# Performance work log

Measured on AMD Instinct MI355X. Metric: run time of the kernel, lower is better.

The kernel has to match this reference:

```python
import jax, jax.numpy as jnp
import numpy as np

B, T, HID = 2, 2048, 2048
NH = 8
D = HID // NH  # head_dim = 256 (expand_ratio=1 so input_dim == hidden_size)
EPS_RMS = 1e-8   # RMSNorm inside BitLinear
EPS_LN = 1e-5    # layernorm_eps for g_norm


def _rms(x, w, eps):
    # weighted RMSNorm over last dim
    return x * jax.lax.rsqrt(jnp.mean(x * x, axis=-1, keepdims=True) + eps) * w


def _act_quant(x):
    # per-token 8-bit fake quant with straight-through estimator
    s = 127.0 / jnp.clip(jnp.max(jnp.abs(x), axis=-1, keepdims=True), 1e-5)
    q = jnp.clip(jnp.round(x * s), -128, 127) / s
    return x + jax.lax.stop_gradient(q - x)


def _weight_quant(w):
    # ternary weight quantization (BitNet b1.58) with STE
    s = 1.0 / jnp.clip(jnp.mean(jnp.abs(w)), 1e-5)
    q = jnp.clip(jnp.round(w * s), -1, 1) / s
    return w + jax.lax.stop_gradient(q - w)


def _bitlinear(x, w, norm_w):
    # FusedBitLinear: RMSNorm -> activation quant -> ternary-weight linear
    xq = _act_quant(_rms(x, norm_w, EPS_RMS))
    return jnp.einsum('btk,ok->bto', xq, _weight_quant(w))


def setup_inputs() -> dict:
    key = jax.random.key(0)
    ks = jax.random.split(key, 5)
    std = 2 ** (-2.5) * np.sqrt(2.0 / (HID + HID))  # xavier_uniform-ish std with gain 2^-2.5
    return {
        'hidden_states': jax.random.normal(ks[0], (B, T, HID), dtype=jnp.float32),
        'w_i': jax.random.normal(ks[1], (HID, HID), dtype=jnp.float32) * std,
        'w_f': jax.random.normal(ks[2], (HID, HID), dtype=jnp.float32) * std,
        'w_g': jax.random.normal(ks[3], (HID, HID), dtype=jnp.float32) * std,
        'w_o': jax.random.normal(ks[4], (HID, HID), dtype=jnp.float32) * std,
        'n_i': jnp.ones((HID,), jnp.float32),
        'n_f': jnp.ones((HID,), jnp.float32),
        'n_g': jnp.ones((HID,), jnp.float32),
        'n_o': jnp.ones((HID,), jnp.float32),
        'gn_w': jnp.ones((HID,), jnp.float32),
    }


def reference(hidden_states, w_i, w_f, w_g, w_o, n_i, n_f, n_g, n_o, gn_w):
    hs = hidden_states
    i = _bitlinear(hs, w_i, n_i)                      # [B,T,HID]
    f = jax.nn.sigmoid(_bitlinear(hs, w_f, n_f))      # forget gate
    # swiglu(i, 1 - f) = silu(i) * (1 - f)
    i = i * jax.nn.sigmoid(i) * (1.0 - f)

    # b l (h d) -> t b h d for scan
    def to_tbhd(x):
        return x.reshape(B, T, NH, D).transpose(1, 0, 2, 3)

    i_t, f_t = to_tbhd(i), to_tbhd(f)

    def step(h, ft_it):
        ft, it = ft_it
        h = ft * h + it
        return h, h

    h0 = jnp.zeros((B, NH, D), dtype=i.dtype)
    _, o = jax.lax.scan(step, h0, (f_t, i_t))         # [T,B,NH,D]
    o = o.transpose(1, 0, 2, 3).reshape(B, T, HID)     # b l (h d)

    # g_norm(g_proj(hs), o): rmsnorm(g) * o * sigmoid(o)
    g = _bitlinear(hs, w_g, n_g)
    o = _rms(g, gn_w, EPS_LN) * o * jax.nn.sigmoid(o)
    return _bitlinear(o, w_o, n_o)
```

## Files before the change

### kernel.cpp

```cpp
#include <hip/hip_runtime.h>
#include <math.h>

#define HID 2048
#define TOKENS 4096
#define TT 2048
#define NCH 4096
#define NC 32
#define CL 64
#define WELEM 4194304

typedef unsigned short u16;
typedef signed char i8;
typedef int i32x4 __attribute__((ext_vector_type(4)));

__device__ inline float sigm(float x) { return 1.0f / (1.0f + expf(-x)); }

__device__ inline float wred_sum(float v) {
#pragma unroll
  for (int o = 32; o > 0; o >>= 1) v += __shfl_down(v, o);
  return v;
}
__device__ inline float wred_max(float v) {
#pragma unroll
  for (int o = 32; o > 0; o >>= 1) v = fmaxf(v, __shfl_down(v, o));
  return v;
}
__device__ inline double wred_sumd(double v) {
#pragma unroll
  for (int o = 32; o > 0; o >>= 1) v += __shfl_down(v, o);
  return v;
}

__device__ __forceinline__ void gl_lds16(const void* g, void* l) {
  __builtin_amdgcn_global_load_lds(
      (__attribute__((address_space(1))) void*)(void*)g,
      (__attribute__((address_space(3))) void*)l, 16, 0, 0);
}

__device__ __forceinline__ int pack8(const int* qi) {
  return (qi[0] & 255) | ((qi[1] & 255) << 8) | ((qi[2] & 255) << 16)
       | ((qi[3] & 255) << 24);
}

__global__ __launch_bounds__(256) void absmean_kernel(
    const float* __restrict__ w0, const float* __restrict__ w1,
    const float* __restrict__ w2, const float* __restrict__ w3,
    double* __restrict__ wsum) {
  int widx = blockIdx.x >> 9;
  int blk = blockIdx.x & 511;
  const float* w = widx == 0 ? w0 : widx == 1 ? w1 : widx == 2 ? w2 : w3;
  size_t base = (size_t)blk * 8192;
  double acc = 0.0;
#pragma unroll
  for (int r = 0; r < 8; ++r) {
    float4 v = *(const float4*)&w[base + (size_t)(r * 256 + threadIdx.x) * 4];
    acc += (double)fabsf(v.x) + (double)fabsf(v.y) + (double)fabsf(v.z) +
           (double)fabsf(v.w);
  }
  acc = wred_sumd(acc);
  __shared__ double sh[4];
  int tid = threadIdx.x;
  if ((tid & 63) == 0) sh[tid >> 6] = acc;
  __syncthreads();
  if (tid == 0) atomicAdd(&wsum[widx], (sh[0] + sh[1]) + (sh[2] + sh[3]));
}

__global__ __launch_bounds__(256) void wquant2_kernel(
    const float* __restrict__ wA, const float* __restrict__ wB,
    const double* __restrict__ wsum, int widxA, int widxB,
    i8* __restrict__ wqA, i8* __restrict__ wqB) {
  int sel = blockIdx.x >> 11;
  int blk = blockIdx.x & 2047;
  const float* w = sel ? wB : wA;
  i8* wq = sel ? wqB : wqA;
  int widx = sel ? widxB : widxA;
  double mean = wsum[widx] * (1.0 / (double)WELEM);
  float s = (float)(1.0 / fmax(mean, 1e-5));
  size_t base = (size_t)blk * 2048 + (size_t)threadIdx.x * 8;
  float4 va = *(const float4*)&w[base];
  float4 vb = *(const float4*)&w[base + 4];
  float vv[8] = {va.x, va.y, va.z, va.w, vb.x, vb.y, vb.z, vb.w};
  int qi[8];
#pragma unroll
  for (int j = 0; j < 8; ++j) {
    float q1 = rintf(vv[j] * s);
    q1 = fminf(fmaxf(q1, -1.0f), 1.0f);
    qi[j] = (int)q1;
  }
  *(int2*)&wq[base] = make_int2(pack8(qi), pack8(qi + 4));
}

__global__ __launch_bounds__(256) void rmsquant_kernel(
    const float* __restrict__ X, const float* __restrict__ nw,
    i8* __restrict__ Xq, float* __restrict__ inv_s) {
  int tok = blockIdx.x;
  int tid = threadIdx.x;
  const float* xrow = X + (size_t)tok * HID;
  int c0 = tid * 8;
  float x[8];
  *(float4*)&x[0] = *(const float4*)&xrow[c0];
  *(float4*)&x[4] = *(const float4*)&xrow[c0 + 4];
  float ss = 0.0f;
#pragma unroll
  for (int j = 0; j < 8; ++j) ss += x[j] * x[j];
  __shared__ float sh[4];
  float v = wred_sum(ss);
  if ((tid & 63) == 0) sh[tid >> 6] = v;
  __syncthreads();
  float tot = (sh[0] + sh[1]) + (sh[2] + sh[3]);
  float rstd = (float)(1.0 / sqrt((double)(tot * (1.0f / HID)) + 1e-8));
  float y[8];
  float amax = 0.0f;
#pragma unroll
  for (int j = 0; j < 8; ++j) {
    y[j] = x[j] * rstd * nw[c0 + j];
    amax = fmaxf(amax, fabsf(y[j]));
  }
  __syncthreads();
  v = wred_max(amax);
  if ((tid & 63) == 0) sh[tid >> 6] = v;
  __syncthreads();
  float am = fmaxf(fmaxf(fmaxf(sh[0], sh[1]), fmaxf(sh[2], sh[3])), 1e-5f);
  float s = 127.0f / am;
  int qi[8];
#pragma unroll
  for (int j = 0; j < 8; ++j) {
    float qq = rintf(y[j] * s);
    qq = fminf(fmaxf(qq, -128.0f), 127.0f);
    qi[j] = (int)qq;
  }
  *(int2*)&Xq[(size_t)tok * HID + c0] = make_int2(pack8(qi), pack8(qi + 4));
  if (tid == 0) inv_s[tok] = am * (1.0f / 127.0f);
}

__global__ __launch_bounds__(256) void rmsquant2_kernel(
    const float* __restrict__ X, const float* __restrict__ nw0,
    const float* __restrict__ nw1, i8* __restrict__ Xq0, i8* __restrict__ Xq1,
    float* __restrict__ inv0, float* __restrict__ inv1) {
  int tok = blockIdx.x;
  int tid = threadIdx.x;
  const float* xrow = X + (size_t)tok * HID;
  int c0 = tid * 8;
  float x[8];
  *(float4*)&x[0] = *(const float4*)&xrow[c0];
  *(float4*)&x[4] = *(const float4*)&xrow[c0 + 4];
  float ss = 0.0f;
#pragma unroll
  for (int j = 0; j < 8; ++j) ss += x[j] * x[j];
  __shared__ float sh[4];
  float v = wred_sum(ss);
  if ((tid & 63) == 0) sh[tid >> 6] = v;
  __syncthreads();
  float tot = (sh[0] + sh[1]) + (sh[2] + sh[3]);
  float rstd = (float)(1.0 / sqrt((double)(tot * (1.0f / HID)) + 1e-8));
#pragma unroll
  for (int pass = 0; pass < 2; ++pass) {
    const float* nw = pass == 0 ? nw0 : nw1;
    i8* Xq = pass == 0 ? Xq0 : Xq1;
    float* inv_s = pass == 0 ? inv0 : inv1;
    float y[8];
    float amax = 0.0f;
#pragma unroll
    for (int j = 0; j < 8; ++j) {
      y[j] = x[j] * rstd * nw[c0 + j];
      amax = fmaxf(amax, fabsf(y[j]));
    }
    __syncthreads();
    float vv = wred_max(amax);
    if ((tid & 63) == 0) sh[tid >> 6] = vv;
    __syncthreads();
    float am = fmaxf(fmaxf(fmaxf(sh[0], sh[1]), fmaxf(sh[2], sh[3])), 1e-5f);
    float s = 127.0f / am;
    int qi[8];
#pragma unroll
    for (int j = 0; j < 8; ++j) {
      float qq = rintf(y[j] * s);
      qq = fminf(fmaxf(qq, -128.0f), 127.0f);
      qi[j] = (int)qq;
    }
    *(int2*)&Xq[(size_t)tok * HID + c0] = make_int2(pack8(qi), pack8(qi + 4));
    if (tid == 0) inv_s[tok] = am * (1.0f / 127.0f);
  }
}

__global__ __launch_bounds__(512) void gemm8_kernel(
    const i8* __restrict__ Aq, const i8* __restrict__ Wq,
    const float* __restrict__ inv_s, const double* __restrict__ wsum, int widx,
    float* __restrict__ Out, int mode) {
  const int tid = threadIdx.x;
  const int lid = blockIdx.x;
  const int swz = (lid & 7) * 64 + (lid >> 3);
  const int n0 = (swz & 15) * 128;
  const int m0 = (swz >> 4) * 128;

  __shared__ __align__(16) i8 As[2][16384];
  __shared__ __align__(16) i8 Bs[2][16384];
  float wscale = (float)fmax(wsum[widx] * (1.0 / (double)WELEM), 1e-5);

  const int wave = tid >> 6, lane = tid & 63;
  const int wm = wave >> 2;
  const int wn = wave & 3;
  const int lrow = lane & 15;
  const int ksel = lane >> 4;
  const int rsw = lrow & 7;
  const int srow8 = lane >> 3;
  const int scol = ((lane & 7) ^ srow8) << 4;

  const i8* Ab = Aq + (size_t)m0 * HID;
  const i8* Wb = Wq + (size_t)n0 * HID;

  i32x4 acc[4][2];
#pragma unroll
  for (int i = 0; i < 4; ++i)
#pragma unroll
    for (int j = 0; j < 2; ++j)
#pragma unroll
      for (int r = 0; r < 4; ++r) acc[i][j][r] = 0;

#define STAGE(buf, k0)                                                      \
  {                                                                         \
    _Pragma("unroll") for (int c = 0; c < 2; ++c) {                         \
      int chunk = wave * 2 + c;                                             \
      int row = chunk * 8 + srow8;                                          \
      gl_lds16(&Ab[(size_t)row * HID + (k0) + scol], &As[buf][chunk * 1024]); \
      gl_lds16(&Wb[(size_t)row * HID + (k0) + scol], &Bs[buf][chunk * 1024]); \
    }                                                                       \
  }

  const int NT = HID / 128;
  STAGE(0, 0)
  __syncthreads();
  int cur = 0;
  for (int kt = 0; kt < NT; ++kt) {
    if (kt + 1 < NT) STAGE(cur ^ 1, (kt + 1) * 128)
    i32x4 af[4][2], bfr[2][2];
#pragma unroll
    for (int i = 0; i < 4; ++i) {
      int ra = wm * 64 + i * 16 + lrow;
#pragma unroll
      for (int kk = 0; kk < 2; ++kk) {
        int phys = ((kk << 2) | ksel) ^ rsw;
        af[i][kk] = *(const i32x4*)&As[cur][ra * 128 + phys * 16];
      }
    }
#pragma unroll
    for (int j = 0; j < 2; ++j) {
      int rb = wn * 32 + j * 16 + lrow;
#pragma unroll
      for (int kk = 0; kk < 2; ++kk) {
        int phys = ((kk << 2) | ksel) ^ rsw;
        bfr[j][kk] = *(const i32x4*)&Bs[cur][rb * 128 + phys * 16];
      }
    }
    __builtin_amdgcn_s_setprio(1);
#pragma unroll
    for (int kk = 0; kk < 2; ++kk)
#pragma unroll
      for (int i = 0; i < 4; ++i)
#pragma unroll
        for (int j = 0; j < 2; ++j)
          acc[i][j] = __builtin_amdgcn_mfma_i32_16x16x64_i8(
              af[i][kk], bfr[j][kk], acc[i][j], 0, 0, 0);
    __builtin_amdgcn_s_setprio(0);
    __syncthreads();
    cur ^= 1;
  }
#undef STAGE

#pragma unroll
  for (int i = 0; i < 4; ++i) {
    int rbase = m0 + wm * 64 + i * 16 + (lane >> 4) * 4;
#pragma unroll
    for (int j = 0; j < 2; ++j) {
      int col = n0 + wn * 32 + j * 16 + lrow;
#pragma unroll
      for (int r = 0; r < 4; ++r) {
        int row = rbase + r;
        float v = (float)acc[i][j][r] * inv_s[row] * wscale;
        size_t oidx = (size_t)row * HID + col;
        if (mode == 0) {
          Out[oidx] = sigm(v);
        } else if (mode == 1) {
          Out[oidx] = v * sigm(v);
        } else {
          Out[oidx] = v;
        }
      }
    }
  }
}

__global__ __launch_bounds__(256) void scan1_kernel(
    const float* __restrict__ F, float* __restrict__ IO, float* __restrict__ P,
    float* __restrict__ H) {
  int c = blockIdx.x * 256 + threadIdx.x;
  int q = blockIdx.y;
  size_t base =
      (size_t)(c >> 11) * TT * HID + (c & 2047) + (size_t)q * CL * HID;
  float h = 0.0f, p = 1.0f;
#pragma unroll 4
  for (int t = 0; t < CL; ++t) {
    size_t idx = base + (size_t)t * HID;
    float f = F[idx];
    float iv = IO[idx];
    h = fmaf(f, h, iv - iv * f);
    p *= f;
    IO[idx] = h;
  }
  P[q * NCH + c] = p;
  H[q * NCH + c] = h;
}

__global__ __launch_bounds__(256) void scan2_kernel(
    const float* __restrict__ P, const float* __restrict__ H,
    float* __restrict__ Ini) {
  int c = blockIdx.x * 256 + threadIdx.x;
  float carry = 0.0f;
#pragma unroll
  for (int q = 0; q < NC; ++q) {
    float pq = P[q * NCH + c];
    float hq = H[q * NCH + c];
    Ini[q * NCH + c] = carry;
    carry = fmaf(pq, carry, hq);
  }
}

__global__ __launch_bounds__(256) void scan3_kernel(
    const float* __restrict__ F, const float* __restrict__ Ini,
    float* __restrict__ IO) {
  int c = blockIdx.x * 256 + threadIdx.x;
  int q = blockIdx.y + 1;
  float h0 = Ini[q * NCH + c];
  if (h0 == 0.0f) return;
  size_t base =
      (size_t)(c >> 11) * TT * HID + (c & 2047) + (size_t)q * CL * HID;
  float p = 1.0f;
#pragma unroll 4
  for (int t = 0; t < CL; ++t) {
    size_t idx = base + (size_t)t * HID;
    p *= F[idx];
    IO[idx] = fmaf(p, h0, IO[idx]);
  }
}

__global__ __launch_bounds__(256) void combine_quant_kernel(
    const float* __restrict__ G, const float* __restrict__ gnw,
    const float* __restrict__ O, const float* __restrict__ nw,
    i8* __restrict__ Xq, float* __restrict__ inv_s) {
  int tok = blockIdx.x;
  int tid = threadIdx.x;
  int c0 = tid * 8;
  const float* grow = G + (size_t)tok * HID;
  const float* orow = O + (size_t)tok * HID;
  float g[8], o[8];
  *(float4*)&g[0] = *(const float4*)&grow[c0];
  *(float4*)&g[4] = *(const float4*)&grow[c0 + 4];
  *(float4*)&o[0] = *(const float4*)&orow[c0];
  *(float4*)&o[4] = *(const float4*)&orow[c0 + 4];
  __shared__ float sh[4];
  float ss = 0.0f;
#pragma unroll
  for (int j = 0; j < 8; ++j) ss += g[j] * g[j];
  float v = wred_sum(ss);
  if ((tid & 63) == 0) sh[tid >> 6] = v;
  __syncthreads();
  float tot = (sh[0] + sh[1]) + (sh[2] + sh[3]);
  float rstd_g = (float)(1.0 / sqrt((double)(tot * (1.0f / HID)) + 1e-5));
  float on[8];
  float ss2 = 0.0f;
#pragma unroll
  for (int j = 0; j < 8; ++j) {
    on[j] = g[j] * rstd_g * gnw[c0 + j] * o[j] * sigm(o[j]);
    ss2 += on[j] * on[j];
  }
  __syncthreads();
  v = wred_sum(ss2);
  if ((tid & 63) == 0) sh[tid >> 6] = v;
  __syncthreads();
  float tot2 = (sh[0] + sh[1]) + (sh[2] + sh[3]);
  float rstd_o = (float)(1.0 / sqrt((double)(tot2 * (1.0f / HID)) + 1e-8));
  float y[8];
  float amax = 0.0f;
#pragma unroll
  for (int j = 0; j < 8; ++j) {
    y[j] = on[j] * rstd_o * nw[c0 + j];
    amax = fmaxf(amax, fabsf(y[j]));
  }
  __syncthreads();
  v = wred_max(amax);
  if ((tid & 63) == 0) sh[tid >> 6] = v;
  __syncthreads();
  float am = fmaxf(fmaxf(fmaxf(sh[0], sh[1]), fmaxf(sh[2], sh[3])), 1e-5f);
  float s = 127.0f / am;
  int qi[8];
#pragma unroll
  for (int j = 0; j < 8; ++j) {
    float qq = rintf(y[j] * s);
    qq = fminf(fmaxf(qq, -128.0f), 127.0f);
    qi[j] = (int)qq;
  }
  *(int2*)&Xq[(size_t)tok * HID + c0] = make_int2(pack8(qi), pack8(qi + 4));
  if (tid == 0) inv_s[tok] = am * (1.0f / 127.0f);
}

extern "C" void kernel_launch(void* const* d_in, const int* in_sizes, int n_in,
                              void* d_out, int out_size, void* d_ws,
                              size_t ws_size, hipStream_t stream) {
  const float* hs = (const float*)d_in[0];
  const float* w_i = (const float*)d_in[1];
  const float* w_f = (const float*)d_in[2];
  const float* w_g = (const float*)d_in[3];
  const float* w_o = (const float*)d_in[4];
  const float* n_i = (const float*)d_in[5];
  const float* n_f = (const float*)d_in[6];
  const float* n_g = (const float*)d_in[7];
  const float* n_o = (const float*)d_in[8];
  const float* gn_w = (const float*)d_in[9];
  float* Out = (float*)d_out;

  char* ws = (char*)d_ws;
  i8* WQ0 = (i8*)ws;
  i8* WQ1 = (i8*)(ws + 4194304);
  i8* XQ0 = (i8*)(ws + 8388608);
  i8* XQ1 = (i8*)(ws + 16777216);
  float* F = (float*)(ws + 25165824);
  float* G = F;
  float* invs0 = (float*)(ws + 58720256);
  float* invs1 = (float*)(ws + 58736640);
  double* wsum = (double*)(ws + 58753024);
  float* scanP = (float*)(ws + 58754048);
  float* scanH = (float*)(ws + 59278336);

  hipMemsetAsync(wsum, 0, 4 * sizeof(double), stream);
  absmean_kernel<<<2048, 256, 0, stream>>>(w_i, w_f, w_g, w_o, wsum);

  wquant2_kernel<<<4096, 256, 0, stream>>>(w_f, w_i, wsum, 1, 0, WQ0, WQ1);
  rmsquant2_kernel<<<TOKENS, 256, 0, stream>>>(hs, n_f, n_i, XQ0, XQ1, invs0,
                                               invs1);

  gemm8_kernel<<<512, 512, 0, stream>>>(XQ0, WQ0, invs0, wsum, 1, F, 0);
  gemm8_kernel<<<512, 512, 0, stream>>>(XQ1, WQ1, invs1, wsum, 0, Out, 1);

  wquant2_kernel<<<4096, 256, 0, stream>>>(w_g, w_o, wsum, 2, 3, WQ0, WQ1);
  rmsquant_kernel<<<TOKENS, 256, 0, stream>>>(hs, n_g, XQ0, invs0);

  scan1_kernel<<<dim3(NCH / 256, NC), 256, 0, stream>>>(F, Out, scanP, scanH);
  scan2_kernel<<<NCH / 256, 256, 0, stream>>>(scanP, scanH, scanP);
  scan3_kernel<<<dim3(NCH / 256, NC - 1), 256, 0, stream>>>(F, scanP, Out);

  gemm8_kernel<<<512, 512, 0, stream>>>(XQ0, WQ0, invs0, wsum, 2, G, 2);

  combine_quant_kernel<<<TOKENS, 256, 0, stream>>>(G, gn_w, Out, n_o, XQ1,
                                                   invs1);

  gemm8_kernel<<<512, 512, 0, stream>>>(XQ1, WQ1, invs1, wsum, 3, Out, 2);
}
```

Baseline: 236.8 us.

## Merge weight/activation quant launches and split GEMM k-tile into two staged phases

All four ternary weight quantizations now run in one launch, and the three input RMSNorm+quant passes run in one kernel, so the hidden-state read happens once and fewer launches are issued. The int8 GEMM main loop is split into two half-phases: each issues half of the next tile's global-to-LDS loads and then runs the MFMAs for one k-slice, using raw barriers with an explicit vmcnt wait in place of __syncthreads. The aim is finer overlap of loads and compute. The cost is a larger workspace and more delicate barrier correctness.

```diff
diff --git a/kernel.cpp b/kernel.cpp
--- a/kernel.cpp
+++ b/kernel.cpp
@@ -65,15 +65,16 @@
   if (tid == 0) atomicAdd(&wsum[widx], (sh[0] + sh[1]) + (sh[2] + sh[3]));
 }
 
-__global__ __launch_bounds__(256) void wquant2_kernel(
-    const float* __restrict__ wA, const float* __restrict__ wB,
-    const double* __restrict__ wsum, int widxA, int widxB,
-    i8* __restrict__ wqA, i8* __restrict__ wqB) {
+__global__ __launch_bounds__(256) void wquant4_kernel(
+    const float* __restrict__ w0, const float* __restrict__ w1,
+    const float* __restrict__ w2, const float* __restrict__ w3,
+    const double* __restrict__ wsum, i8* __restrict__ q0, i8* __restrict__ q1,
+    i8* __restrict__ q2, i8* __restrict__ q3) {
   int sel = blockIdx.x >> 11;
   int blk = blockIdx.x & 2047;
-  const float* w = sel ? wB : wA;
-  i8* wq = sel ? wqB : wqA;
-  int widx = sel ? widxB : widxA;
+  const float* w = sel == 0 ? w0 : sel == 1 ? w1 : sel == 2 ? w2 : w3;
+  i8* wq = sel == 0 ? q0 : sel == 1 ? q1 : sel == 2 ? q2 : q3;
+  int widx = sel == 0 ? 1 : sel == 1 ? 0 : sel;
   double mean = wsum[widx] * (1.0 / (double)WELEM);
   float s = (float)(1.0 / fmax(mean, 1e-5));
   size_t base = (size_t)blk * 2048 + (size_t)threadIdx.x * 8;
@@ -83,16 +84,19 @@
   int qi[8];
 #pragma unroll
   for (int j = 0; j < 8; ++j) {
-    float q1 = rintf(vv[j] * s);
-    q1 = fminf(fmaxf(q1, -1.0f), 1.0f);
-    qi[j] = (int)q1;
+    float q1v = rintf(vv[j] * s);
+    q1v = fminf(fmaxf(q1v, -1.0f), 1.0f);
+    qi[j] = (int)q1v;
   }
   *(int2*)&wq[base] = make_int2(pack8(qi), pack8(qi + 4));
 }
 
-__global__ __launch_bounds__(256) void rmsquant_kernel(
-    const float* __restrict__ X, const float* __restrict__ nw,
-    i8* __restrict__ Xq, float* __restrict__ inv_s) {
+__global__ __launch_bounds__(256) void rmsquant3_kernel(
+    const float* __restrict__ X, const float* __restrict__ nw0,
+    const float* __restrict__ nw1, const float* __restrict__ nw2,
+    i8* __restrict__ Xq0, i8* __restrict__ Xq1, i8* __restrict__ Xq2,
+    float* __restrict__ inv0, float* __restrict__ inv1,
+    float* __restrict__ inv2) {
   int tok = blockIdx.x;
   int tid = threadIdx.x;
   const float* xrow = X + (size_t)tok * HID;
@@ -109,55 +113,11 @@
   __syncthreads();
   float tot = (sh[0] + sh[1]) + (sh[2] + sh[3]);
   float rstd = (float)(1.0 / sqrt((double)(tot * (1.0f / HID)) + 1e-8));
-  float y[8];
-  float amax = 0.0f;
-#pragma unroll
-  for (int j = 0; j < 8; ++j) {
-    y[j] = x[j] * rstd * nw[c0 + j];
-    amax = fmaxf(amax, fabsf(y[j]));
-  }
-  __syncthreads();
-  v = wred_max(amax);
-  if ((tid & 63) == 0) sh[tid >> 6] = v;
-  __syncthreads();
-  float am = fmaxf(fmaxf(fmaxf(sh[0], sh[1]), fmaxf(sh[2], sh[3])), 1e-5f);
-  float s = 127.0f / am;
-  int qi[8];
-#pragma unroll
-  for (int j = 0; j < 8; ++j) {
-    float qq = rintf(y[j] * s);
-    qq = fminf(fmaxf(qq, -128.0f), 127.0f);
-    qi[j] = (int)qq;
-  }
-  *(int2*)&Xq[(size_t)tok * HID + c0] = make_int2(pack8(qi), pack8(qi + 4));
-  if (tid == 0) inv_s[tok] = am * (1.0f / 127.0f);
-}
-
-__global__ __launch_bounds__(256) void rmsquant2_kernel(
-    const float* __restrict__ X, const float* __restrict__ nw0,
-    const float* __restrict__ nw1, i8* __restrict__ Xq0, i8* __restrict__ Xq1,
-    float* __restrict__ inv0, float* __restrict__ inv1) {
-  int tok = blockIdx.x;
-  int tid = threadIdx.x;
-  const float* xrow = X + (size_t)tok * HID;
-  int c0 = tid * 8;
-  float x[8];
-  *(float4*)&x[0] = *(const float4*)&xrow[c0];
-  *(float4*)&x[4] = *(const float4*)&xrow[c0 + 4];
-  float ss = 0.0f;
-#pragma unroll
-  for (int j = 0; j < 8; ++j) ss += x[j] * x[j];
-  __shared__ float sh[4];
-  float v = wred_sum(ss);
-  if ((tid & 63) == 0) sh[tid >> 6] = v;
-  __syncthreads();
-  float tot = (sh[0] + sh[1]) + (sh[2] + sh[3]);
-  float rstd = (float)(1.0 / sqrt((double)(tot * (1.0f / HID)) + 1e-8));
-#pragma unroll
-  for (int pass = 0; pass < 2; ++pass) {
-    const float* nw = pass == 0 ? nw0 : nw1;
-    i8* Xq = pass == 0 ? Xq0 : Xq1;
-    float* inv_s = pass == 0 ? inv0 : inv1;
+#pragma unroll
+  for (int pass = 0; pass < 3; ++pass) {
+    const float* nw = pass == 0 ? nw0 : pass == 1 ? nw1 : nw2;
+    i8* Xq = pass == 0 ? Xq0 : pass == 1 ? Xq1 : Xq2;
+    float* inv_s = pass == 0 ? inv0 : pass == 1 ? inv1 : inv2;
     float y[8];
     float amax = 0.0f;
 #pragma unroll
@@ -217,55 +177,51 @@
 #pragma unroll
       for (int r = 0; r < 4; ++r) acc[i][j][r] = 0;
 
-#define STAGE(buf, k0)                                                      \
+#define STAGEH(buf, k0, h)                                                  \
   {                                                                         \
-    _Pragma("unroll") for (int c = 0; c < 2; ++c) {                         \
-      int chunk = wave * 2 + c;                                             \
-      int row = chunk * 8 + srow8;                                          \
-      gl_lds16(&Ab[(size_t)row * HID + (k0) + scol], &As[buf][chunk * 1024]); \
-      gl_lds16(&Wb[(size_t)row * HID + (k0) + scol], &Bs[buf][chunk * 1024]); \
+    int chunk = wave * 2 + (h);                                             \
+    int row = chunk * 8 + srow8;                                            \
+    gl_lds16(&Ab[(size_t)row * HID + (k0) + scol], &As[buf][chunk * 1024]); \
+    gl_lds16(&Wb[(size_t)row * HID + (k0) + scol], &Bs[buf][chunk * 1024]); \
+  }
+
+#define PHASE(buf, ks)                                                      \
+  {                                                                         \
+    i32x4 af[4], bfr[2];                                                    \
+    _Pragma("unroll") for (int i = 0; i < 4; ++i) {                         \
+      int ra = wm * 64 + i * 16 + lrow;                                     \
+      int phys = (((ks) << 2) | ksel) ^ rsw;                                \
+      af[i] = *(const i32x4*)&As[buf][ra * 128 + phys * 16];                \
     }                                                                       \
+    _Pragma("unroll") for (int j = 0; j < 2; ++j) {                         \
+      int rb = wn * 32 + j * 16 + lrow;                                     \
+      int phys = (((ks) << 2) | ksel) ^ rsw;                                \
+      bfr[j] = *(const i32x4*)&Bs[buf][rb * 128 + phys * 16];               \
+    }                                                                       \
+    __builtin_amdgcn_s_setprio(1);                                          \
+    _Pragma("unroll") for (int i = 0; i < 4; ++i)                           \
+        _Pragma("unroll") for (int j = 0; j < 2; ++j) acc[i][j] =           \
+            __builtin_amdgcn_mfma_i32_16x16x64_i8(af[i], bfr[j], acc[i][j], \
+                                                  0, 0, 0);                 \
+    __builtin_amdgcn_s_setprio(0);                                          \
   }
 
   const int NT = HID / 128;
-  STAGE(0, 0)
-  __syncthreads();
+  STAGEH(0, 0, 0)
+  STAGEH(0, 0, 1)
   int cur = 0;
   for (int kt = 0; kt < NT; ++kt) {
-    if (kt + 1 < NT) STAGE(cur ^ 1, (kt + 1) * 128)
-    i32x4 af[4][2], bfr[2][2];
-#pragma unroll
-    for (int i = 0; i < 4; ++i) {
-      int ra = wm * 64 + i * 16 + lrow;
-#pragma unroll
-      for (int kk = 0; kk < 2; ++kk) {
-        int phys = ((kk << 2) | ksel) ^ rsw;
-        af[i][kk] = *(const i32x4*)&As[cur][ra * 128 + phys * 16];
-      }
-    }
-#pragma unroll
-    for (int j = 0; j < 2; ++j) {
-      int rb = wn * 32 + j * 16 + lrow;
-#pragma unroll
-      for (int kk = 0; kk < 2; ++kk) {
-        int phys = ((kk << 2) | ksel) ^ rsw;
-        bfr[j][kk] = *(const i32x4*)&Bs[cur][rb * 128 + phys * 16];
-      }
-    }
-    __builtin_amdgcn_s_setprio(1);
-#pragma unroll
-    for (int kk = 0; kk < 2; ++kk)
-#pragma unroll
-      for (int i = 0; i < 4; ++i)
-#pragma unroll
-        for (int j = 0; j < 2; ++j)
-          acc[i][j] = __builtin_amdgcn_mfma_i32_16x16x64_i8(
-              af[i][kk], bfr[j][kk], acc[i][j], 0, 0, 0);
-    __builtin_amdgcn_s_setprio(0);
-    __syncthreads();
+    asm volatile("s_waitcnt vmcnt(0)" ::: "memory");
+    __builtin_amdgcn_s_barrier();
+    if (kt + 1 < NT) STAGEH(cur ^ 1, (kt + 1) * 128, 0)
+    PHASE(cur, 0)
+    __builtin_amdgcn_s_barrier();
+    if (kt + 1 < NT) STAGEH(cur ^ 1, (kt + 1) * 128, 1)
+    PHASE(cur, 1)
     cur ^= 1;
   }
-#undef STAGE
+#undef STAGEH
+#undef PHASE
 
 #pragma unroll
   for (int i = 0; i < 4; ++i) {
@@ -421,37 +377,39 @@
   char* ws = (char*)d_ws;
   i8* WQ0 = (i8*)ws;
   i8* WQ1 = (i8*)(ws + 4194304);
-  i8* XQ0 = (i8*)(ws + 8388608);
-  i8* XQ1 = (i8*)(ws + 16777216);
-  float* F = (float*)(ws + 25165824);
+  i8* WQ2 = (i8*)(ws + 8388608);
+  i8* WQ3 = (i8*)(ws + 12582912);
+  i8* XQ0 = (i8*)(ws + 16777216);
+  i8* XQ1 = (i8*)(ws + 25165824);
+  i8* XQ2 = (i8*)(ws + 33554432);
+  float* F = (float*)(ws + 41943040);
   float* G = F;
-  float* invs0 = (float*)(ws + 58720256);
-  float* invs1 = (float*)(ws + 58736640);
-  double* wsum = (double*)(ws + 58753024);
-  float* scanP = (float*)(ws + 58754048);
-  float* scanH = (float*)(ws + 59278336);
+  float* invs0 = (float*)(ws + 75497472);
+  float* invs1 = (float*)(ws + 75513856);
+  float* invs2 = (float*)(ws + 75530240);
+  double* wsum = (double*)(ws + 75546624);
+  float* scanP = (float*)(ws + 75547648);
+  float* scanH = (float*)(ws + 76071936);
 
   hipMemsetAsync(wsum, 0, 4 * sizeof(double), stream);
   absmean_kernel<<<2048, 256, 0, stream>>>(w_i, w_f, w_g, w_o, wsum);
 
-  wquant2_kernel<<<4096, 256, 0, stream>>>(w_f, w_i, wsum, 1, 0, WQ0, WQ1);
-  rmsquant2_kernel<<<TOKENS, 256, 0, stream>>>(hs, n_f, n_i, XQ0, XQ1, invs0,
-                                               invs1);
+  wquant4_kernel<<<8192, 256, 0, stream>>>(w_f, w_i, w_g, w_o, wsum, WQ0, WQ1,
+                                           WQ2, WQ3);
+  rmsquant3_kernel<<<TOKENS, 256, 0, stream>>>(hs, n_f, n_i, n_g, XQ0, XQ1,
+                                               XQ2, invs0, invs1, invs2);
 
   gemm8_kernel<<<512, 512, 0, stream>>>(XQ0, WQ0, invs0, wsum, 1, F, 0);
   gemm8_kernel<<<512, 512, 0, stream>>>(XQ1, WQ1, invs1, wsum, 0, Out, 1);
-
-  wquant2_kernel<<<4096, 256, 0, stream>>>(w_g, w_o, wsum, 2, 3, WQ0, WQ1);
-  rmsquant_kernel<<<TOKENS, 256, 0, stream>>>(hs, n_g, XQ0, invs0);
 
   scan1_kernel<<<dim3(NCH / 256, NC), 256, 0, stream>>>(F, Out, scanP, scanH);
   scan2_kernel<<<NCH / 256, 256, 0, stream>>>(scanP, scanH, scanP);
   scan3_kernel<<<dim3(NCH / 256, NC - 1), 256, 0, stream>>>(F, scanP, Out);
 
-  gemm8_kernel<<<512, 512, 0, stream>>>(XQ0, WQ0, invs0, wsum, 2, G, 2);
-
-  combine_quant_kernel<<<TOKENS, 256, 0, stream>>>(G, gn_w, Out, n_o, XQ1,
-                                                   invs1);
-
-  gemm8_kernel<<<512, 512, 0, stream>>>(XQ1, WQ1, invs1, wsum, 3, Out, 2);
-}
+  gemm8_kernel<<<512, 512, 0, stream>>>(XQ2, WQ2, invs2, wsum, 2, G, 2);
+
+  combine_quant_kernel<<<TOKENS, 256, 0, stream>>>(G, gn_w, Out, n_o, XQ0,
+                                                   invs0);
+
+  gemm8_kernel<<<512, 512, 0, stream>>>(XQ0, WQ3, invs0, wsum, 3, Out, 2);
+}
```

After: 239.7 us. About the same (+1.2%).
